# Optimization experiments

Measured on AMD Instinct MI355X. Metric: run time of the kernel, lower is better.

Reference implementation:

```python
import jax, jax.numpy as jnp
import numpy as np

B, C, L = 16, 384, 4096      # batch, in_channels, sequence length
K = 4096                     # kernel_size (global 'same'-size kernel)
KH = 32                      # kernel_hidden_channels
NL = 3                       # kernel_no_layers
OMEGA = 976.0                # omega_0
HID = 384                    # net hidden_channels (pointwise out)


def setup_inputs() -> dict:
    key = jax.random.key(0)
    ks = jax.random.split(key, 10)
    s = 1.0 / np.sqrt(KH)
    return {
        "x": jax.random.normal(ks[0], (B, C, L), jnp.float32),
        # Gaussian mask parameters (learnable, init mean=0 sigma=1)
        "mask_mean": jnp.zeros((1,), jnp.float32),
        "mask_sigma": jnp.ones((1,), jnp.float32),
        # MAGNet (MFN with anisotropic Gabor filters): NL+1 filters
        "gabor_freq_w": jax.random.normal(ks[1], (NL + 1, KH, 1), jnp.float32),
        "gabor_freq_b": jax.random.uniform(ks[2], (NL + 1, KH), jnp.float32, -np.pi, np.pi),
        "gabor_gamma": jax.random.gamma(ks[3], 2.0, (NL + 1, KH, 1)).astype(jnp.float32),
        "gabor_mu": jax.random.uniform(ks[4], (NL + 1, KH, 1), jnp.float32, -1.0, 1.0),
        # NL hidden linear layers of the MFN
        "lin_w": jax.random.normal(ks[5], (NL, KH, KH), jnp.float32) * s,
        "lin_b": jnp.zeros((NL, KH), jnp.float32),
        # output linear layer (re-weighted by 1/sqrt(C*K) in forward)
        "out_w": jax.random.normal(ks[6], (C, KH), jnp.float32) * s,
        "out_b": jnp.zeros((C,), jnp.float32),
        # pointwise (1x1) conv weight, bias=False per net_cfg
        "pw_w": jax.random.normal(ks[7], (HID, C), jnp.float32) * (1.0 / np.sqrt(C)),
    }


def reference(x, mask_mean, mask_sigma, gabor_freq_w, gabor_freq_b,
              gabor_gamma, gabor_mu, lin_w, lin_b, out_w, out_b, pw_w):
    # relative positions in [-1, 1], shape [K, 1] (data_dim = 1)
    pos = jnp.linspace(-1.0, 1.0, K, dtype=x.dtype).reshape(K, 1)

    def gabor(i):
        # anisotropic Gabor filter: gaussian envelope * sinusoid
        diff = pos[:, None, :] - gabor_mu[i][None]                    # [K, KH, 1]
        env = jnp.exp(-0.5 * jnp.sum((gabor_gamma[i][None] * diff) ** 2, -1))  # [K, KH]
        sinus = jnp.sin(OMEGA * (pos @ gabor_freq_w[i].T) + gabor_freq_b[i])   # [K, KH]
        return env * sinus

    # MFN forward over kernel positions
    h = gabor(0)
    for i in range(NL):  # fixed small layer count
        h = (h @ lin_w[i].T + lin_b[i]) * gabor(i + 1)
    # re_weight_output_layer: scale output so kernel variance ~ 1/(C*K)
    scale = 1.0 / np.sqrt(C * K)
    conv_kernel = ((h @ out_w.T + out_b) * scale).T[None]             # [1, C, K]

    # learnable gaussian mask over positions -> masked kernel
    mask = jnp.exp(-0.5 * ((pos[:, 0] - mask_mean[0]) / mask_sigma[0]) ** 2)  # [K]
    masked_kernel = conv_kernel * mask[None, None, :]

    # causal FFT long convolution (K > fft_threshold -> fftconv path)
    n = L + K  # linear (non-circular) convolution length
    y = jnp.fft.irfft(jnp.fft.rfft(x, n=n) * jnp.fft.rfft(masked_kernel, n=n), n=n)[..., :L]

    # pointwise 1x1 conv, bias=False
    out = jnp.einsum('bcl,oc->bol', y, pw_w)
    return out
```

## Files before the change

### kernel.cpp

```cpp
#include <hip/hip_runtime.h>
#include <math.h>

#define B_    16
#define C_    384
#define L_    4096
#define K_    4096
#define KH_   32
#define NL_   3
#define HID_  384
#define NFFT  8192
#define OMEGA_ 976.0f

#define SWZ(a) ((a) ^ ((((a) >> 7) & 1) << 4))

__global__ __launch_bounds__(256) void gen_tw(float2* __restrict__ tw) {
  int j = blockIdx.x * 256 + threadIdx.x;
  if (j < NFFT) {
    double a = -2.0 * 3.14159265358979323846 * (double)j / (double)NFFT;
    double s, c;
    sincos(a, &s, &c);
    tw[j] = make_float2((float)c, (float)s);
  }
}

__device__ __forceinline__ float2 cadd(float2 a, float2 b) { return make_float2(a.x + b.x, a.y + b.y); }
__device__ __forceinline__ float2 csub(float2 a, float2 b) { return make_float2(a.x - b.x, a.y - b.y); }
__device__ __forceinline__ float2 cmul(float2 a, float2 b) { return make_float2(a.x * b.x - a.y * b.y, a.x * b.y + a.y * b.x); }
__device__ __forceinline__ float2 cmulc(float2 a, float2 b) {
  return make_float2(a.x * b.x + a.y * b.y, a.y * b.x - a.x * b.y);
}

__device__ __forceinline__ void dft8_fwd(float2* a) {
  const float c = 0.70710678118654752f;
  float2 t0 = cadd(a[0], a[4]), t1 = csub(a[0], a[4]);
  float2 t2 = cadd(a[2], a[6]), t3 = csub(a[2], a[6]);
  float2 t4 = cadd(a[1], a[5]), t5 = csub(a[1], a[5]);
  float2 t6 = cadd(a[3], a[7]), t7 = csub(a[3], a[7]);
  float2 E0 = cadd(t0, t2), E2 = csub(t0, t2);
  float2 E1 = make_float2(t1.x + t3.y, t1.y - t3.x);
  float2 E3 = make_float2(t1.x - t3.y, t1.y + t3.x);
  float2 O0 = cadd(t4, t6), O2 = csub(t4, t6);
  float2 O1 = make_float2(t5.x + t7.y, t5.y - t7.x);
  float2 O3 = make_float2(t5.x - t7.y, t5.y + t7.x);
  float2 O1w = make_float2(c * (O1.x + O1.y), c * (O1.y - O1.x));
  float2 O2w = make_float2(O2.y, -O2.x);
  float2 O3w = make_float2(c * (O3.y - O3.x), -c * (O3.x + O3.y));
  a[0] = cadd(E0, O0);  a[4] = csub(E0, O0);
  a[1] = cadd(E1, O1w); a[5] = csub(E1, O1w);
  a[2] = cadd(E2, O2w); a[6] = csub(E2, O2w);
  a[3] = cadd(E3, O3w); a[7] = csub(E3, O3w);
}

__device__ __forceinline__ void dft8_inv(float2* a) {
  const float c = 0.70710678118654752f;
  float2 t0 = cadd(a[0], a[4]), t1 = csub(a[0], a[4]);
  float2 t2 = cadd(a[2], a[6]), t3 = csub(a[2], a[6]);
  float2 t4 = cadd(a[1], a[5]), t5 = csub(a[1], a[5]);
  float2 t6 = cadd(a[3], a[7]), t7 = csub(a[3], a[7]);
  float2 E0 = cadd(t0, t2), E2 = csub(t0, t2);
  float2 E1 = make_float2(t1.x - t3.y, t1.y + t3.x);
  float2 E3 = make_float2(t1.x + t3.y, t1.y - t3.x);
  float2 O0 = cadd(t4, t6), O2 = csub(t4, t6);
  float2 O1 = make_float2(t5.x - t7.y, t5.y + t7.x);
  float2 O3 = make_float2(t5.x + t7.y, t5.y - t7.x);
  float2 O1w = make_float2(c * (O1.x - O1.y), c * (O1.x + O1.y));
  float2 O2w = make_float2(-O2.y, O2.x);
  float2 O3w = make_float2(-c * (O3.x + O3.y), c * (O3.x - O3.y));
  a[0] = cadd(E0, O0);  a[4] = csub(E0, O0);
  a[1] = cadd(E1, O1w); a[5] = csub(E1, O1w);
  a[2] = cadd(E2, O2w); a[6] = csub(E2, O2w);
  a[3] = cadd(E3, O3w); a[7] = csub(E3, O3w);
}

template <bool INV>
__device__ __forceinline__ void stage8(float* zr, float* zi, const float2* __restrict__ tw,
                                       int tid, int d, int ld, int stride) {
  #pragma unroll
  for (int rep = 0; rep < 4; ++rep) {
    int idx = tid + rep * 256;
    int j = idx & (d - 1);
    int p = ((idx >> ld) << (ld + 3)) + j;
    float2 v[8];
    #pragma unroll
    for (int t = 0; t < 8; ++t) { int q = SWZ(p + t * d); v[t] = make_float2(zr[q], zi[q]); }
    if (INV) {
      #pragma unroll
      for (int k = 1; k < 8; ++k) v[k] = cmulc(v[k], tw[j * k * stride]);
      dft8_inv(v);
    } else {
      dft8_fwd(v);
      #pragma unroll
      for (int k = 1; k < 8; ++k) v[k] = cmul(v[k], tw[j * k * stride]);
    }
    #pragma unroll
    for (int t = 0; t < 8; ++t) { int q = SWZ(p + t * d); zr[q] = v[t].x; zi[q] = v[t].y; }
  }
  __syncthreads();
}

__device__ __forceinline__ void reg16_fwd(float2* v, const float2* __restrict__ tw) {
  float2 t[8];
  #pragma unroll
  for (int k = 0; k < 8; ++k) t[k] = v[2 * k];
  dft8_fwd(t);
  #pragma unroll
  for (int k = 0; k < 8; ++k) v[2 * k] = t[k];
  #pragma unroll
  for (int k = 0; k < 8; ++k) t[k] = v[2 * k + 1];
  dft8_fwd(t);
  #pragma unroll
  for (int k = 1; k < 8; ++k) t[k] = cmul(t[k], tw[k * 512]);
  #pragma unroll
  for (int k = 0; k < 8; ++k) v[2 * k + 1] = t[k];
  #pragma unroll
  for (int q = 0; q < 8; ++q) {
    float2 a = v[2 * q], b = v[2 * q + 1];
    v[2 * q] = cadd(a, b); v[2 * q + 1] = csub(a, b);
  }
}

__device__ __forceinline__ void reg16_inv(float2* v, const float2* __restrict__ tw) {
  #pragma unroll
  for (int q = 0; q < 8; ++q) {
    float2 a = v[2 * q], b = v[2 * q + 1];
    v[2 * q] = cadd(a, b); v[2 * q + 1] = csub(a, b);
  }
  float2 t[8];
  #pragma unroll
  for (int k = 0; k < 8; ++k) t[k] = v[2 * k];
  dft8_inv(t);
  #pragma unroll
  for (int k = 0; k < 8; ++k) v[2 * k] = t[k];
  #pragma unroll
  for (int k = 0; k < 8; ++k) t[k] = cmulc(v[2 * k + 1], tw[k * 512]);
  dft8_inv(t);
  #pragma unroll
  for (int k = 0; k < 8; ++k) v[2 * k + 1] = t[k];
}

__global__ __launch_bounds__(256) void gen_mk(
    const float* __restrict__ mask_mean, const float* __restrict__ mask_sigma,
    const float* __restrict__ gfw, const float* __restrict__ gfb,
    const float* __restrict__ gg,  const float* __restrict__ gmu,
    const float* __restrict__ lin_w, const float* __restrict__ lin_b,
    const float* __restrict__ out_w, const float* __restrict__ out_b,
    float* __restrict__ mk) {
  const int t = threadIdx.x;
  const int k = blockIdx.x * 256 + t;
  const int c0 = blockIdx.y * 16;
  const float xp = -1.0f + 2.0f * (float)k / (float)(K_ - 1);

  float h[KH_];
  #pragma unroll
  for (int j = 0; j < KH_; ++j) {
    float d   = gg[j] * (xp - gmu[j]);
    float env = expf(-0.5f * d * d);
    float su  = sinf(OMEGA_ * (xp * gfw[j]) + gfb[j]);
    h[j] = env * su;
  }
  for (int i = 0; i < NL_; ++i) {
    const float* lw = lin_w + i * KH_ * KH_;
    const int go = (i + 1) * KH_;
    float nh[KH_];
    #pragma unroll
    for (int h2 = 0; h2 < KH_; ++h2) {
      float acc = lin_b[i * KH_ + h2];
      #pragma unroll
      for (int j = 0; j < KH_; ++j) acc = fmaf(h[j], lw[h2 * KH_ + j], acc);
      float d   = gg[go + h2] * (xp - gmu[go + h2]);
      float env = expf(-0.5f * d * d);
      float su  = sinf(OMEGA_ * (xp * gfw[go + h2]) + gfb[go + h2]);
      nh[h2] = acc * (env * su);
    }
    #pragma unroll
    for (int j = 0; j < KH_; ++j) h[j] = nh[j];
  }
  float mw = (xp - mask_mean[0]) / mask_sigma[0];
  float ms = expf(-0.5f * mw * mw) * rsqrtf((float)(C_ * K_));
  #pragma unroll
  for (int j = 0; j < KH_; ++j) h[j] *= ms;

  for (int cc = 0; cc < 16; ++cc) {
    int c = c0 + cc;
    float acc = out_b[c] * ms;
    #pragma unroll
    for (int j = 0; j < KH_; ++j) acc = fmaf(h[j], out_w[c * KH_ + j], acc);
    mk[(size_t)c * K_ + k] = acc;
  }
}

__global__ __launch_bounds__(256) void fft_h(const float* __restrict__ mk,
                                             const float2* __restrict__ tw,
                                             float2* __restrict__ Hspec) {
  extern __shared__ float smem[];
  float* zr = smem;
  float* zi = smem + NFFT;
  const int c = blockIdx.x;
  const int tid = threadIdx.x;
  const float4* row4 = reinterpret_cast<const float4*>(mk + (size_t)c * K_);
  const float4 z4 = make_float4(0.f, 0.f, 0.f, 0.f);
  for (int i = tid; i < K_ / 4; i += 256) {
    int p = i * 4;
    *reinterpret_cast<float4*>(&zr[SWZ(p)]) = row4[i];
    *reinterpret_cast<float4*>(&zi[SWZ(p)]) = z4;
    *reinterpret_cast<float4*>(&zr[SWZ(p + K_)]) = z4;
    *reinterpret_cast<float4*>(&zi[SWZ(p + K_)]) = z4;
  }
  __syncthreads();
  stage8<false>(zr, zi, tw, tid, 1024, 10, 1);
  stage8<false>(zr, zi, tw, tid, 128, 7, 8);
  stage8<false>(zr, zi, tw, tid, 16, 4, 64);

  const float inv = 1.0f / (float)NFFT;
  float2* outp = Hspec + (size_t)c * NFFT;
  #pragma unroll
  for (int rep = 0; rep < 2; ++rep) {
    int cb = tid + rep * 256;
    int base = cb * 16, pb = SWZ(base);
    float2 v[16];
    #pragma unroll
    for (int q4 = 0; q4 < 4; ++q4) {
      float4 re = *reinterpret_cast<const float4*>(&zr[pb + q4 * 4]);
      float4 im = *reinterpret_cast<const float4*>(&zi[pb + q4 * 4]);
      v[q4 * 4 + 0] = make_float2(re.x, im.x);
      v[q4 * 4 + 1] = make_float2(re.y, im.y);
      v[q4 * 4 + 2] = make_float2(re.z, im.z);
      v[q4 * 4 + 3] = make_float2(re.w, im.w);
    }
    reg16_fwd(v, tw);
    #pragma unroll
    for (int q = 0; q < 16; ++q) outp[base + q] = make_float2(v[q].x * inv, v[q].y * inv);
  }
}

__global__ __launch_bounds__(256) void fft_conv(const float* __restrict__ x,
                                                const float2* __restrict__ Hspec,
                                                const float2* __restrict__ tw,
                                                float* __restrict__ y) {
  extern __shared__ float smem[];
  float* zr = smem;
  float* zi = smem + NFFT;
  const int c  = blockIdx.x % C_;
  const int pr = blockIdx.x / C_;
  const int b1 = 2 * pr, b2 = b1 + 1;
  const int tid = threadIdx.x;
  const float4* x1 = reinterpret_cast<const float4*>(x + ((size_t)b1 * C_ + c) * L_);
  const float4* x2 = reinterpret_cast<const float4*>(x + ((size_t)b2 * C_ + c) * L_);
  const float4 z4 = make_float4(0.f, 0.f, 0.f, 0.f);
  for (int i = tid; i < L_ / 4; i += 256) {
    int p = i * 4;
    *reinterpret_cast<float4*>(&zr[SWZ(p)]) = x1[i];
    *reinterpret_cast<float4*>(&zi[SWZ(p)]) = x2[i];
    *reinterpret_cast<float4*>(&zr[SWZ(p + L_)]) = z4;
    *reinterpret_cast<float4*>(&zi[SWZ(p + L_)]) = z4;
  }
  __syncthreads();
  stage8<false>(zr, zi, tw, tid, 1024, 10, 1);
  stage8<false>(zr, zi, tw, tid, 128, 7, 8);
  stage8<false>(zr, zi, tw, tid, 16, 4, 64);

  const float2* Hc = Hspec + (size_t)c * NFFT;
  #pragma unroll
  for (int rep = 0; rep < 2; ++rep) {
    int cb = tid + rep * 256;
    int base = cb * 16, pb = SWZ(base);
    float2 v[16];
    #pragma unroll
    for (int q4 = 0; q4 < 4; ++q4) {
      float4 re = *reinterpret_cast<const float4*>(&zr[pb + q4 * 4]);
      float4 im = *reinterpret_cast<const float4*>(&zi[pb + q4 * 4]);
      v[q4 * 4 + 0] = make_float2(re.x, im.x);
      v[q4 * 4 + 1] = make_float2(re.y, im.y);
      v[q4 * 4 + 2] = make_float2(re.z, im.z);
      v[q4 * 4 + 3] = make_float2(re.w, im.w);
    }
    reg16_fwd(v, tw);
    #pragma unroll
    for (int q = 0; q < 16; ++q) v[q] = cmul(v[q], Hc[base + q]);
    reg16_inv(v, tw);
    #pragma unroll
    for (int q4 = 0; q4 < 4; ++q4) {
      float4 re = make_float4(v[q4 * 4 + 0].x, v[q4 * 4 + 1].x, v[q4 * 4 + 2].x, v[q4 * 4 + 3].x);
      float4 im = make_float4(v[q4 * 4 + 0].y, v[q4 * 4 + 1].y, v[q4 * 4 + 2].y, v[q4 * 4 + 3].y);
      *reinterpret_cast<float4*>(&zr[pb + q4 * 4]) = re;
      *reinterpret_cast<float4*>(&zi[pb + q4 * 4]) = im;
    }
  }
  __syncthreads();
  stage8<true>(zr, zi, tw, tid, 16, 4, 64);
  stage8<true>(zr, zi, tw, tid, 128, 7, 8);
  stage8<true>(zr, zi, tw, tid, 1024, 10, 1);

  float4* y1 = reinterpret_cast<float4*>(y + ((size_t)b1 * C_ + c) * L_);
  float4* y2 = reinterpret_cast<float4*>(y + ((size_t)b2 * C_ + c) * L_);
  for (int i = tid; i < L_ / 4; i += 256) {
    int p = i * 4;
    y1[i] = *reinterpret_cast<const float4*>(&zr[SWZ(p)]);
    y2[i] = *reinterpret_cast<const float4*>(&zi[SWZ(p)]);
  }
}

#define MT 128
#define NT 128
#define KT 16
#define LDT 132
__global__ __launch_bounds__(256) void pw_gemm(const float* __restrict__ y,
                                               const float* __restrict__ pw,
                                               float* __restrict__ out) {
  const int b  = blockIdx.z;
  const int m0 = blockIdx.y * MT;
  const int n0 = blockIdx.x * NT;
  __shared__ float As[KT][LDT];
  __shared__ float Bs[KT][LDT];
  const int tid = threadIdx.x;
  const int tx = tid & 15, ty = tid >> 4;
  float acc[2][2][4][4] = {{{{0.f}}}};
  const float* yb = y + (size_t)b * C_ * L_;

  for (int k0 = 0; k0 < C_; k0 += KT) {
    #pragma unroll
    for (int rep = 0; rep < 2; ++rep) {
      int idx = tid + rep * 256;
      int row = idx >> 2, c4 = (idx & 3) << 2;
      float4 av = *reinterpret_cast<const float4*>(pw + (size_t)(m0 + row) * C_ + k0 + c4);
      As[c4 + 0][row] = av.x; As[c4 + 1][row] = av.y;
      As[c4 + 2][row] = av.z; As[c4 + 3][row] = av.w;
    }
    #pragma unroll
    for (int rep = 0; rep < 2; ++rep) {
      int idx = tid + rep * 256;
      int r = idx >> 5, cc = (idx & 31) << 2;
      float4 bv = *reinterpret_cast<const float4*>(yb + (size_t)(k0 + r) * L_ + n0 + cc);
      *reinterpret_cast<float4*>(&Bs[r][cc]) = bv;
    }
    __syncthreads();
    #pragma unroll
    for (int kk = 0; kk < KT; ++kk) {
      float4 a0 = *reinterpret_cast<const float4*>(&As[kk][ty * 4]);
      float4 a1 = *reinterpret_cast<const float4*>(&As[kk][ty * 4 + 64]);
      float4 b0 = *reinterpret_cast<const float4*>(&Bs[kk][tx * 4]);
      float4 b1 = *reinterpret_cast<const float4*>(&Bs[kk][tx * 4 + 64]);
      float av[2][4] = {{a0.x, a0.y, a0.z, a0.w}, {a1.x, a1.y, a1.z, a1.w}};
      float bv[2][4] = {{b0.x, b0.y, b0.z, b0.w}, {b1.x, b1.y, b1.z, b1.w}};
      #pragma unroll
      for (int ri = 0; ri < 2; ++ri)
        #pragma unroll
        for (int rj = 0; rj < 2; ++rj)
          #pragma unroll
          for (int i = 0; i < 4; ++i)
            #pragma unroll
            for (int j = 0; j < 4; ++j)
              acc[ri][rj][i][j] = fmaf(av[ri][i], bv[rj][j], acc[ri][rj][i][j]);
    }
    __syncthreads();
  }
  #pragma unroll
  for (int ri = 0; ri < 2; ++ri)
    #pragma unroll
    for (int i = 0; i < 4; ++i) {
      int grow = m0 + ty * 4 + i + ri * 64;
      float* orow = out + ((size_t)b * HID_ + grow) * L_ + n0;
      #pragma unroll
      for (int rj = 0; rj < 2; ++rj) {
        float4 v = make_float4(acc[ri][rj][i][0], acc[ri][rj][i][1],
                               acc[ri][rj][i][2], acc[ri][rj][i][3]);
        *reinterpret_cast<float4*>(orow + tx * 4 + rj * 64) = v;
      }
    }
}

extern "C" void kernel_launch(void* const* d_in, const int* in_sizes, int n_in,
                              void* d_out, int out_size, void* d_ws, size_t ws_size,
                              hipStream_t stream) {
  (void)in_sizes; (void)n_in; (void)out_size; (void)ws_size;
  const float* x          = (const float*)d_in[0];
  const float* mask_mean  = (const float*)d_in[1];
  const float* mask_sigma = (const float*)d_in[2];
  const float* gfw        = (const float*)d_in[3];
  const float* gfb        = (const float*)d_in[4];
  const float* gg         = (const float*)d_in[5];
  const float* gmu        = (const float*)d_in[6];
  const float* lin_w      = (const float*)d_in[7];
  const float* lin_b      = (const float*)d_in[8];
  const float* out_w      = (const float*)d_in[9];
  const float* out_b      = (const float*)d_in[10];
  const float* pw_w       = (const float*)d_in[11];
  float* out = (float*)d_out;

  char* ws = (char*)d_ws;
  float2* tw = (float2*)ws;
  float*  mk = (float*)(ws + 65536);
  float2* Hs = (float2*)(ws + 65536 + 6291456);
  float*  y  = (float*)(ws + 65536 + 6291456 + 25165824);

  gen_tw<<<NFFT / 256, 256, 0, stream>>>(tw);
  gen_mk<<<dim3(K_ / 256, 24), 256, 0, stream>>>(mask_mean, mask_sigma, gfw, gfb, gg, gmu,
                                                 lin_w, lin_b, out_w, out_b, mk);
  fft_h<<<C_, 256, 2 * NFFT * sizeof(float), stream>>>(mk, tw, Hs);
  fft_conv<<<(B_ / 2) * C_, 256, 2 * NFFT * sizeof(float), stream>>>(x, Hs, tw, y);
  pw_gemm<<<dim3(L_ / NT, HID_ / MT, B_), 256, 0, stream>>>(y, pw_w, out);
}
```

Baseline: 844.7 us.

## Use 512-thread FFT blocks with paired butterflies and register-prefetch GEMM loads

The FFT kernels move to 512 threads per block. Each thread now runs one radix-8 butterfly on two adjacent columns at once, using float2 LDS accesses and a packed real/imag layout, instead of four sequential butterflies. The register radix-16 pass rotates its float4 access order per thread to spread LDS bank traffic. The pointwise GEMM prefetches the next K-tile into registers while computing the current one. This trades more threads and register pressure for fewer LDS instructions and better latency hiding.

```diff
diff --git a/kernel.cpp b/kernel.cpp
--- a/kernel.cpp
+++ b/kernel.cpp
@@ -30,70 +30,95 @@
   return make_float2(a.x * b.x + a.y * b.y, a.y * b.x - a.x * b.y);
 }
 
-__device__ __forceinline__ void dft8_fwd(float2* a) {
+struct cp { float2 re, im; };
+__device__ __forceinline__ float2 f2a(float2 a, float2 b) { return make_float2(a.x + b.x, a.y + b.y); }
+__device__ __forceinline__ float2 f2s(float2 a, float2 b) { return make_float2(a.x - b.x, a.y - b.y); }
+__device__ __forceinline__ float2 f2m(float2 a, float2 b) { return make_float2(a.x * b.x, a.y * b.y); }
+__device__ __forceinline__ float2 f2k(float2 a, float s)  { return make_float2(a.x * s, a.y * s); }
+__device__ __forceinline__ cp cpadd(cp a, cp b) { return {f2a(a.re, b.re), f2a(a.im, b.im)}; }
+__device__ __forceinline__ cp cpsub(cp a, cp b) { return {f2s(a.re, b.re), f2s(a.im, b.im)}; }
+__device__ __forceinline__ cp cpmul(cp a, float2 wr, float2 wi) {
+  return { f2s(f2m(a.re, wr), f2m(a.im, wi)), f2a(f2m(a.re, wi), f2m(a.im, wr)) };
+}
+__device__ __forceinline__ cp cpmulc(cp a, float2 wr, float2 wi) {
+  return { f2a(f2m(a.re, wr), f2m(a.im, wi)), f2s(f2m(a.im, wr), f2m(a.re, wi)) };
+}
+
+__device__ __forceinline__ void dft8p_fwd(cp* a) {
   const float c = 0.70710678118654752f;
-  float2 t0 = cadd(a[0], a[4]), t1 = csub(a[0], a[4]);
-  float2 t2 = cadd(a[2], a[6]), t3 = csub(a[2], a[6]);
-  float2 t4 = cadd(a[1], a[5]), t5 = csub(a[1], a[5]);
-  float2 t6 = cadd(a[3], a[7]), t7 = csub(a[3], a[7]);
-  float2 E0 = cadd(t0, t2), E2 = csub(t0, t2);
-  float2 E1 = make_float2(t1.x + t3.y, t1.y - t3.x);
-  float2 E3 = make_float2(t1.x - t3.y, t1.y + t3.x);
-  float2 O0 = cadd(t4, t6), O2 = csub(t4, t6);
-  float2 O1 = make_float2(t5.x + t7.y, t5.y - t7.x);
-  float2 O3 = make_float2(t5.x - t7.y, t5.y + t7.x);
-  float2 O1w = make_float2(c * (O1.x + O1.y), c * (O1.y - O1.x));
-  float2 O2w = make_float2(O2.y, -O2.x);
-  float2 O3w = make_float2(c * (O3.y - O3.x), -c * (O3.x + O3.y));
-  a[0] = cadd(E0, O0);  a[4] = csub(E0, O0);
-  a[1] = cadd(E1, O1w); a[5] = csub(E1, O1w);
-  a[2] = cadd(E2, O2w); a[6] = csub(E2, O2w);
-  a[3] = cadd(E3, O3w); a[7] = csub(E3, O3w);
-}
-
-__device__ __forceinline__ void dft8_inv(float2* a) {
+  cp t0 = cpadd(a[0], a[4]), t1 = cpsub(a[0], a[4]);
+  cp t2 = cpadd(a[2], a[6]), t3 = cpsub(a[2], a[6]);
+  cp t4 = cpadd(a[1], a[5]), t5 = cpsub(a[1], a[5]);
+  cp t6 = cpadd(a[3], a[7]), t7 = cpsub(a[3], a[7]);
+  cp E0 = cpadd(t0, t2), E2 = cpsub(t0, t2);
+  cp E1 = { f2a(t1.re, t3.im), f2s(t1.im, t3.re) };
+  cp E3 = { f2s(t1.re, t3.im), f2a(t1.im, t3.re) };
+  cp O0 = cpadd(t4, t6), O2 = cpsub(t4, t6);
+  cp O1 = { f2a(t5.re, t7.im), f2s(t5.im, t7.re) };
+  cp O3 = { f2s(t5.re, t7.im), f2a(t5.im, t7.re) };
+  cp O1w = { f2k(f2a(O1.re, O1.im), c), f2k(f2s(O1.im, O1.re), c) };
+  cp O2w = { O2.im, f2k(O2.re, -1.f) };
+  cp O3w = { f2k(f2s(O3.im, O3.re), c), f2k(f2a(O3.re, O3.im), -c) };
+  a[0] = cpadd(E0, O0);  a[4] = cpsub(E0, O0);
+  a[1] = cpadd(E1, O1w); a[5] = cpsub(E1, O1w);
+  a[2] = cpadd(E2, O2w); a[6] = cpsub(E2, O2w);
+  a[3] = cpadd(E3, O3w); a[7] = cpsub(E3, O3w);
+}
+
+__device__ __forceinline__ void dft8p_inv(cp* a) {
   const float c = 0.70710678118654752f;
-  float2 t0 = cadd(a[0], a[4]), t1 = csub(a[0], a[4]);
-  float2 t2 = cadd(a[2], a[6]), t3 = csub(a[2], a[6]);
-  float2 t4 = cadd(a[1], a[5]), t5 = csub(a[1], a[5]);
-  float2 t6 = cadd(a[3], a[7]), t7 = csub(a[3], a[7]);
-  float2 E0 = cadd(t0, t2), E2 = csub(t0, t2);
-  float2 E1 = make_float2(t1.x - t3.y, t1.y + t3.x);
-  float2 E3 = make_float2(t1.x + t3.y, t1.y - t3.x);
-  float2 O0 = cadd(t4, t6), O2 = csub(t4, t6);
-  float2 O1 = make_float2(t5.x - t7.y, t5.y + t7.x);
-  float2 O3 = make_float2(t5.x + t7.y, t5.y - t7.x);
-  float2 O1w = make_float2(c * (O1.x - O1.y), c * (O1.x + O1.y));
-  float2 O2w = make_float2(-O2.y, O2.x);
-  float2 O3w = make_float2(-c * (O3.x + O3.y), c * (O3.x - O3.y));
-  a[0] = cadd(E0, O0);  a[4] = csub(E0, O0);
-  a[1] = cadd(E1, O1w); a[5] = csub(E1, O1w);
-  a[2] = cadd(E2, O2w); a[6] = csub(E2, O2w);
-  a[3] = cadd(E3, O3w); a[7] = csub(E3, O3w);
+  cp t0 = cpadd(a[0], a[4]), t1 = cpsub(a[0], a[4]);
+  cp t2 = cpadd(a[2], a[6]), t3 = cpsub(a[2], a[6]);
+  cp t4 = cpadd(a[1], a[5]), t5 = cpsub(a[1], a[5]);
+  cp t6 = cpadd(a[3], a[7]), t7 = cpsub(a[3], a[7]);
+  cp E0 = cpadd(t0, t2), E2 = cpsub(t0, t2);
+  cp E1 = { f2s(t1.re, t3.im), f2a(t1.im, t3.re) };
+  cp E3 = { f2a(t1.re, t3.im), f2s(t1.im, t3.re) };
+  cp O0 = cpadd(t4, t6), O2 = cpsub(t4, t6);
+  cp O1 = { f2s(t5.re, t7.im), f2a(t5.im, t7.re) };
+  cp O3 = { f2a(t5.re, t7.im), f2s(t5.im, t7.re) };
+  cp O1w = { f2k(f2s(O1.re, O1.im), c), f2k(f2a(O1.re, O1.im), c) };
+  cp O2w = { f2k(O2.im, -1.f), O2.re };
+  cp O3w = { f2k(f2a(O3.re, O3.im), -c), f2k(f2s(O3.re, O3.im), c) };
+  a[0] = cpadd(E0, O0);  a[4] = cpsub(E0, O0);
+  a[1] = cpadd(E1, O1w); a[5] = cpsub(E1, O1w);
+  a[2] = cpadd(E2, O2w); a[6] = cpsub(E2, O2w);
+  a[3] = cpadd(E3, O3w); a[7] = cpsub(E3, O3w);
 }
 
 template <bool INV>
-__device__ __forceinline__ void stage8(float* zr, float* zi, const float2* __restrict__ tw,
-                                       int tid, int d, int ld, int stride) {
-  #pragma unroll
-  for (int rep = 0; rep < 4; ++rep) {
-    int idx = tid + rep * 256;
-    int j = idx & (d - 1);
-    int p = ((idx >> ld) << (ld + 3)) + j;
-    float2 v[8];
-    #pragma unroll
-    for (int t = 0; t < 8; ++t) { int q = SWZ(p + t * d); v[t] = make_float2(zr[q], zi[q]); }
-    if (INV) {
-      #pragma unroll
-      for (int k = 1; k < 8; ++k) v[k] = cmulc(v[k], tw[j * k * stride]);
-      dft8_inv(v);
-    } else {
-      dft8_fwd(v);
-      #pragma unroll
-      for (int k = 1; k < 8; ++k) v[k] = cmul(v[k], tw[j * k * stride]);
-    }
-    #pragma unroll
-    for (int t = 0; t < 8; ++t) { int q = SWZ(p + t * d); zr[q] = v[t].x; zi[q] = v[t].y; }
+__device__ __forceinline__ void stage8p(float* zr, float* zi, const float2* __restrict__ tw,
+                                        int tid, int d, int ld, int stride) {
+  const int i2 = tid * 2;
+  const int j  = i2 & (d - 1);
+  const int p  = ((i2 >> ld) << (ld + 3)) + j;
+  cp v[8];
+  #pragma unroll
+  for (int t = 0; t < 8; ++t) {
+    int q = SWZ(p + t * d);
+    v[t].re = *reinterpret_cast<const float2*>(&zr[q]);
+    v[t].im = *reinterpret_cast<const float2*>(&zi[q]);
+  }
+  if (INV) {
+    #pragma unroll
+    for (int k = 1; k < 8; ++k) {
+      float2 wA = tw[j * k * stride], wB = tw[(j + 1) * k * stride];
+      v[k] = cpmulc(v[k], make_float2(wA.x, wB.x), make_float2(wA.y, wB.y));
+    }
+    dft8p_inv(v);
+  } else {
+    dft8p_fwd(v);
+    #pragma unroll
+    for (int k = 1; k < 8; ++k) {
+      float2 wA = tw[j * k * stride], wB = tw[(j + 1) * k * stride];
+      v[k] = cpmul(v[k], make_float2(wA.x, wB.x), make_float2(wA.y, wB.y));
+    }
+  }
+  #pragma unroll
+  for (int t = 0; t < 8; ++t) {
+    int q = SWZ(p + t * d);
+    *reinterpret_cast<float2*>(&zr[q]) = v[t].re;
+    *reinterpret_cast<float2*>(&zi[q]) = v[t].im;
   }
   __syncthreads();
 }
@@ -102,12 +127,50 @@
   float2 t[8];
   #pragma unroll
   for (int k = 0; k < 8; ++k) t[k] = v[2 * k];
-  dft8_fwd(t);
+  {
+    const float c = 0.70710678118654752f;
+    float2 t0 = cadd(t[0], t[4]), t1 = csub(t[0], t[4]);
+    float2 t2 = cadd(t[2], t[6]), t3 = csub(t[2], t[6]);
+    float2 t4 = cadd(t[1], t[5]), t5 = csub(t[1], t[5]);
+    float2 t6 = cadd(t[3], t[7]), t7 = csub(t[3], t[7]);
+    float2 E0 = cadd(t0, t2), E2 = csub(t0, t2);
+    float2 E1 = make_float2(t1.x + t3.y, t1.y - t3.x);
+    float2 E3 = make_float2(t1.x - t3.y, t1.y + t3.x);
+    float2 O0 = cadd(t4, t6), O2 = csub(t4, t6);
+    float2 O1 = make_float2(t5.x + t7.y, t5.y - t7.x);
+    float2 O3 = make_float2(t5.x - t7.y, t5.y + t7.x);
+    float2 O1w = make_float2(c * (O1.x + O1.y), c * (O1.y - O1.x));
+    float2 O2w = make_float2(O2.y, -O2.x);
+    float2 O3w = make_float2(c * (O3.y - O3.x), -c * (O3.x + O3.y));
+    t[0] = cadd(E0, O0);  t[4] = csub(E0, O0);
+    t[1] = cadd(E1, O1w); t[5] = csub(E1, O1w);
+    t[2] = cadd(E2, O2w); t[6] = csub(E2, O2w);
+    t[3] = cadd(E3, O3w); t[7] = csub(E3, O3w);
+  }
   #pragma unroll
   for (int k = 0; k < 8; ++k) v[2 * k] = t[k];
   #pragma unroll
   for (int k = 0; k < 8; ++k) t[k] = v[2 * k + 1];
-  dft8_fwd(t);
+  {
+    const float c = 0.70710678118654752f;
+    float2 t0 = cadd(t[0], t[4]), t1 = csub(t[0], t[4]);
+    float2 t2 = cadd(t[2], t[6]), t3 = csub(t[2], t[6]);
+    float2 t4 = cadd(t[1], t[5]), t5 = csub(t[1], t[5]);
+    float2 t6 = cadd(t[3], t[7]), t7 = csub(t[3], t[7]);
+    float2 E0 = cadd(t0, t2), E2 = csub(t0, t2);
+    float2 E1 = make_float2(t1.x + t3.y, t1.y - t3.x);
+    float2 E3 = make_float2(t1.x - t3.y, t1.y + t3.x);
+    float2 O0 = cadd(t4, t6), O2 = csub(t4, t6);
+    float2 O1 = make_float2(t5.x + t7.y, t5.y - t7.x);
+    float2 O3 = make_float2(t5.x - t7.y, t5.y + t7.x);
+    float2 O1w = make_float2(c * (O1.x + O1.y), c * (O1.y - O1.x));
+    float2 O2w = make_float2(O2.y, -O2.x);
+    float2 O3w = make_float2(c * (O3.y - O3.x), -c * (O3.x + O3.y));
+    t[0] = cadd(E0, O0);  t[4] = csub(E0, O0);
+    t[1] = cadd(E1, O1w); t[5] = csub(E1, O1w);
+    t[2] = cadd(E2, O2w); t[6] = csub(E2, O2w);
+    t[3] = cadd(E3, O3w); t[7] = csub(E3, O3w);
+  }
   #pragma unroll
   for (int k = 1; k < 8; ++k) t[k] = cmul(t[k], tw[k * 512]);
   #pragma unroll
@@ -128,12 +191,50 @@
   float2 t[8];
   #pragma unroll
   for (int k = 0; k < 8; ++k) t[k] = v[2 * k];
-  dft8_inv(t);
+  {
+    const float c = 0.70710678118654752f;
+    float2 t0 = cadd(t[0], t[4]), t1 = csub(t[0], t[4]);
+    float2 t2 = cadd(t[2], t[6]), t3 = csub(t[2], t[6]);
+    float2 t4 = cadd(t[1], t[5]), t5 = csub(t[1], t[5]);
+    float2 t6 = cadd(t[3], t[7]), t7 = csub(t[3], t[7]);
+    float2 E0 = cadd(t0, t2), E2 = csub(t0, t2);
+    float2 E1 = make_float2(t1.x - t3.y, t1.y + t3.x);
+    float2 E3 = make_float2(t1.x + t3.y, t1.y - t3.x);
+    float2 O0 = cadd(t4, t6), O2 = csub(t4, t6);
+    float2 O1 = make_float2(t5.x - t7.y, t5.y + t7.x);
+    float2 O3 = make_float2(t5.x + t7.y, t5.y - t7.x);
+    float2 O1w = make_float2(c * (O1.x - O1.y), c * (O1.x + O1.y));
+    float2 O2w = make_float2(-O2.y, O2.x);
+    float2 O3w = make_float2(-c * (O3.x + O3.y), c * (O3.x - O3.y));
+    t[0] = cadd(E0, O0);  t[4] = csub(E0, O0);
+    t[1] = cadd(E1, O1w); t[5] = csub(E1, O1w);
+    t[2] = cadd(E2, O2w); t[6] = csub(E2, O2w);
+    t[3] = cadd(E3, O3w); t[7] = csub(E3, O3w);
+  }
   #pragma unroll
   for (int k = 0; k < 8; ++k) v[2 * k] = t[k];
   #pragma unroll
   for (int k = 0; k < 8; ++k) t[k] = cmulc(v[2 * k + 1], tw[k * 512]);
-  dft8_inv(t);
+  {
+    const float c = 0.70710678118654752f;
+    float2 t0 = cadd(t[0], t[4]), t1 = csub(t[0], t[4]);
+    float2 t2 = cadd(t[2], t[6]), t3 = csub(t[2], t[6]);
+    float2 t4 = cadd(t[1], t[5]), t5 = csub(t[1], t[5]);
+    float2 t6 = cadd(t[3], t[7]), t7 = csub(t[3], t[7]);
+    float2 E0 = cadd(t0, t2), E2 = csub(t0, t2);
+    float2 E1 = make_float2(t1.x - t3.y, t1.y + t3.x);
+    float2 E3 = make_float2(t1.x + t3.y, t1.y - t3.x);
+    float2 O0 = cadd(t4, t6), O2 = csub(t4, t6);
+    float2 O1 = make_float2(t5.x - t7.y, t5.y + t7.x);
+    float2 O3 = make_float2(t5.x + t7.y, t5.y - t7.x);
+    float2 O1w = make_float2(c * (O1.x - O1.y), c * (O1.x + O1.y));
+    float2 O2w = make_float2(-O2.y, O2.x);
+    float2 O3w = make_float2(-c * (O3.x + O3.y), c * (O3.x - O3.y));
+    t[0] = cadd(E0, O0);  t[4] = csub(E0, O0);
+    t[1] = cadd(E1, O1w); t[5] = csub(E1, O1w);
+    t[2] = cadd(E2, O2w); t[6] = csub(E2, O2w);
+    t[3] = cadd(E3, O3w); t[7] = csub(E3, O3w);
+  }
   #pragma unroll
   for (int k = 0; k < 8; ++k) v[2 * k + 1] = t[k];
 }
@@ -189,9 +290,9 @@
   }
 }
 
-__global__ __launch_bounds__(256) void fft_h(const float* __restrict__ mk,
-                                             const float2* __restrict__ tw,
-                                             float2* __restrict__ Hspec) {
+__global__ __launch_bounds__(512, 4) void fft_h(const float* __restrict__ mk,
+                                                const float2* __restrict__ tw,
+                                                float2* __restrict__ Hspec) {
   extern __shared__ float smem[];
   float* zr = smem;
   float* zi = smem + NFFT;
@@ -199,7 +300,7 @@
   const int tid = threadIdx.x;
   const float4* row4 = reinterpret_cast<const float4*>(mk + (size_t)c * K_);
   const float4 z4 = make_float4(0.f, 0.f, 0.f, 0.f);
-  for (int i = tid; i < K_ / 4; i += 256) {
+  for (int i = tid; i < K_ / 4; i += 512) {
     int p = i * 4;
     *reinterpret_cast<float4*>(&zr[SWZ(p)]) = row4[i];
     *reinterpret_cast<float4*>(&zi[SWZ(p)]) = z4;
@@ -207,19 +308,20 @@
     *reinterpret_cast<float4*>(&zi[SWZ(p + K_)]) = z4;
   }
   __syncthreads();
-  stage8<false>(zr, zi, tw, tid, 1024, 10, 1);
-  stage8<false>(zr, zi, tw, tid, 128, 7, 8);
-  stage8<false>(zr, zi, tw, tid, 16, 4, 64);
+  stage8p<false>(zr, zi, tw, tid, 1024, 10, 1);
+  stage8p<false>(zr, zi, tw, tid, 128, 7, 8);
+  stage8p<false>(zr, zi, tw, tid, 16, 4, 64);
 
   const float inv = 1.0f / (float)NFFT;
   float2* outp = Hspec + (size_t)c * NFFT;
-  #pragma unroll
-  for (int rep = 0; rep < 2; ++rep) {
-    int cb = tid + rep * 256;
-    int base = cb * 16, pb = SWZ(base);
+  {
+    const int base = tid * 16;
+    const int pb = SWZ(base);
+    const int rot = tid & 3;
     float2 v[16];
     #pragma unroll
-    for (int q4 = 0; q4 < 4; ++q4) {
+    for (int iq = 0; iq < 4; ++iq) {
+      int q4 = (iq + rot) & 3;
       float4 re = *reinterpret_cast<const float4*>(&zr[pb + q4 * 4]);
       float4 im = *reinterpret_cast<const float4*>(&zi[pb + q4 * 4]);
       v[q4 * 4 + 0] = make_float2(re.x, im.x);
@@ -233,10 +335,10 @@
   }
 }
 
-__global__ __launch_bounds__(256) void fft_conv(const float* __restrict__ x,
-                                                const float2* __restrict__ Hspec,
-                                                const float2* __restrict__ tw,
-                                                float* __restrict__ y) {
+__global__ __launch_bounds__(512, 4) void fft_conv(const float* __restrict__ x,
+                                                   const float2* __restrict__ Hspec,
+                                                   const float2* __restrict__ tw,
+                                                   float* __restrict__ y) {
   extern __shared__ float smem[];
   float* zr = smem;
   float* zi = smem + NFFT;
@@ -247,7 +349,7 @@
   const float4* x1 = reinterpret_cast<const float4*>(x + ((size_t)b1 * C_ + c) * L_);
   const float4* x2 = reinterpret_cast<const float4*>(x + ((size_t)b2 * C_ + c) * L_);
   const float4 z4 = make_float4(0.f, 0.f, 0.f, 0.f);
-  for (int i = tid; i < L_ / 4; i += 256) {
+  for (int i = tid; i < L_ / 4; i += 512) {
     int p = i * 4;
     *reinterpret_cast<float4*>(&zr[SWZ(p)]) = x1[i];
     *reinterpret_cast<float4*>(&zi[SWZ(p)]) = x2[i];
@@ -255,18 +357,19 @@
     *reinterpret_cast<float4*>(&zi[SWZ(p + L_)]) = z4;
   }
   __syncthreads();
-  stage8<false>(zr, zi, tw, tid, 1024, 10, 1);
-  stage8<false>(zr, zi, tw, tid, 128, 7, 8);
-  stage8<false>(zr, zi, tw, tid, 16, 4, 64);
+  stage8p<false>(zr, zi, tw, tid, 1024, 10, 1);
+  stage8p<false>(zr, zi, tw, tid, 128, 7, 8);
+  stage8p<false>(zr, zi, tw, tid, 16, 4, 64);
 
   const float2* Hc = Hspec + (size_t)c * NFFT;
-  #pragma unroll
-  for (int rep = 0; rep < 2; ++rep) {
-    int cb = tid + rep * 256;
-    int base = cb * 16, pb = SWZ(base);
+  {
+    const int base = tid * 16;
+    const int pb = SWZ(base);
+    const int rot = tid & 3;
     float2 v[16];
     #pragma unroll
-    for (int q4 = 0; q4 < 4; ++q4) {
+    for (int iq = 0; iq < 4; ++iq) {
+      int q4 = (iq + rot) & 3;
       float4 re = *reinterpret_cast<const float4*>(&zr[pb + q4 * 4]);
       float4 im = *reinterpret_cast<const float4*>(&zi[pb + q4 * 4]);
       v[q4 * 4 + 0] = make_float2(re.x, im.x);
@@ -279,7 +382,8 @@
     for (int q = 0; q < 16; ++q) v[q] = cmul(v[q], Hc[base + q]);
     reg16_inv(v, tw);
     #pragma unroll
-    for (int q4 = 0; q4 < 4; ++q4) {
+    for (int iq = 0; iq < 4; ++iq) {
+      int q4 = (iq + rot) & 3;
       float4 re = make_float4(v[q4 * 4 + 0].x, v[q4 * 4 + 1].x, v[q4 * 4 + 2].x, v[q4 * 4 + 3].x);
       float4 im = make_float4(v[q4 * 4 + 0].y, v[q4 * 4 + 1].y, v[q4 * 4 + 2].y, v[q4 * 4 + 3].y);
       *reinterpret_cast<float4*>(&zr[pb + q4 * 4]) = re;
@@ -287,13 +391,13 @@
     }
   }
   __syncthreads();
-  stage8<true>(zr, zi, tw, tid, 16, 4, 64);
-  stage8<true>(zr, zi, tw, tid, 128, 7, 8);
-  stage8<true>(zr, zi, tw, tid, 1024, 10, 1);
+  stage8p<true>(zr, zi, tw, tid, 16, 4, 64);
+  stage8p<true>(zr, zi, tw, tid, 128, 7, 8);
+  stage8p<true>(zr, zi, tw, tid, 1024, 10, 1);
 
   float4* y1 = reinterpret_cast<float4*>(y + ((size_t)b1 * C_ + c) * L_);
   float4* y2 = reinterpret_cast<float4*>(y + ((size_t)b2 * C_ + c) * L_);
-  for (int i = tid; i < L_ / 4; i += 256) {
+  for (int i = tid; i < L_ / 4; i += 512) {
     int p = i * 4;
     y1[i] = *reinterpret_cast<const float4*>(&zr[SWZ(p)]);
     y2[i] = *reinterpret_cast<const float4*>(&zi[SWZ(p)]);
@@ -304,9 +408,9 @@
 #define NT 128
 #define KT 16
 #define LDT 132
-__global__ __launch_bounds__(256) void pw_gemm(const float* __restrict__ y,
-                                               const float* __restrict__ pw,
-                                               float* __restrict__ out) {
+__global__ __launch_bounds__(256, 4) void pw_gemm(const float* __restrict__ y,
+                                                  const float* __restrict__ pw,
+                                                  float* __restrict__ out) {
   const int b  = blockIdx.z;
   const int m0 = blockIdx.y * MT;
   const int n0 = blockIdx.x * NT;
@@ -314,26 +418,33 @@
   __shared__ float Bs[KT][LDT];
   const int tid = threadIdx.x;
   const int tx = tid & 15, ty = tid >> 4;
+  const int arow = tid >> 2, ac4 = (tid & 3) << 2;
+  const int brow = tid >> 5, bcc = (tid & 31) << 2;
   float acc[2][2][4][4] = {{{{0.f}}}};
   const float* yb = y + (size_t)b * C_ * L_;
 
+  float4 pa[2], pbv[2];
+  #pragma unroll
+  for (int rep = 0; rep < 2; ++rep) {
+    pa[rep]  = *reinterpret_cast<const float4*>(pw + (size_t)(m0 + arow + rep * 64) * C_ + ac4);
+    pbv[rep] = *reinterpret_cast<const float4*>(yb + (size_t)(brow + rep * 8) * L_ + n0 + bcc);
+  }
   for (int k0 = 0; k0 < C_; k0 += KT) {
     #pragma unroll
     for (int rep = 0; rep < 2; ++rep) {
-      int idx = tid + rep * 256;
-      int row = idx >> 2, c4 = (idx & 3) << 2;
-      float4 av = *reinterpret_cast<const float4*>(pw + (size_t)(m0 + row) * C_ + k0 + c4);
-      As[c4 + 0][row] = av.x; As[c4 + 1][row] = av.y;
-      As[c4 + 2][row] = av.z; As[c4 + 3][row] = av.w;
-    }
-    #pragma unroll
-    for (int rep = 0; rep < 2; ++rep) {
-      int idx = tid + rep * 256;
-      int r = idx >> 5, cc = (idx & 31) << 2;
-      float4 bv = *reinterpret_cast<const float4*>(yb + (size_t)(k0 + r) * L_ + n0 + cc);
-      *reinterpret_cast<float4*>(&Bs[r][cc]) = bv;
+      int row = arow + rep * 64;
+      As[ac4 + 0][row] = pa[rep].x; As[ac4 + 1][row] = pa[rep].y;
+      As[ac4 + 2][row] = pa[rep].z; As[ac4 + 3][row] = pa[rep].w;
+      *reinterpret_cast<float4*>(&Bs[brow + rep * 8][bcc]) = pbv[rep];
     }
     __syncthreads();
+    if (k0 + KT < C_) {
+      #pragma unroll
+      for (int rep = 0; rep < 2; ++rep) {
+        pa[rep]  = *reinterpret_cast<const float4*>(pw + (size_t)(m0 + arow + rep * 64) * C_ + (k0 + KT) + ac4);
+        pbv[rep] = *reinterpret_cast<const float4*>(yb + (size_t)(k0 + KT + brow + rep * 8) * L_ + n0 + bcc);
+      }
+    }
     #pragma unroll
     for (int kk = 0; kk < KT; ++kk) {
       float4 a0 = *reinterpret_cast<const float4*>(&As[kk][ty * 4]);
@@ -396,7 +507,7 @@
   gen_tw<<<NFFT / 256, 256, 0, stream>>>(tw);
   gen_mk<<<dim3(K_ / 256, 24), 256, 0, stream>>>(mask_mean, mask_sigma, gfw, gfb, gg, gmu,
                                                  lin_w, lin_b, out_w, out_b, mk);
-  fft_h<<<C_, 256, 2 * NFFT * sizeof(float), stream>>>(mk, tw, Hs);
-  fft_conv<<<(B_ / 2) * C_, 256, 2 * NFFT * sizeof(float), stream>>>(x, Hs, tw, y);
+  fft_h<<<C_, 512, 2 * NFFT * sizeof(float), stream>>>(mk, tw, Hs);
+  fft_conv<<<(B_ / 2) * C_, 512, 2 * NFFT * sizeof(float), stream>>>(x, Hs, tw, y);
   pw_gemm<<<dim3(L_ / NT, HID_ / MT, B_), 256, 0, stream>>>(y, pw_w, out);
 }
```

Measured after the change: 1.694 ms. +100.6%, slower.
